# Kernel optimization log

Hardware: AMD Instinct MI355X
Metric: run time of the kernel (lower is better)

The kernel has to match this reference:

```python
import jax, jax.numpy as jnp
import numpy as np

B, IMG, P, D, E, K, H = 32, 224, 16, 512, 8, 2, 8
G = IMG // P
T = G * G          # 196 patches
PD = P * P         # 256 patch dim
FF = 4 * D         # expert hidden

def _posenc(t, d):
    pos = jnp.arange(t, dtype=jnp.float32)[:, None]
    i = jnp.arange(0, d, 2, dtype=jnp.float32)
    ang = pos / jnp.power(10000.0, i / d)
    pe = jnp.zeros((t, d), jnp.float32)
    pe = pe.at[:, 0::2].set(jnp.sin(ang))
    pe = pe.at[:, 1::2].set(jnp.cos(ang))
    return pe

def _attn(x, Wq, Wk, Wv, Wo, bo):
    bs, t, d = x.shape
    hs = d // H
    q = (x @ Wq).reshape(bs, t, H, hs).transpose(0, 2, 1, 3)
    k = (x @ Wk).reshape(bs, t, H, hs).transpose(0, 2, 1, 3)
    v = (x @ Wv).reshape(bs, t, H, hs).transpose(0, 2, 1, 3)
    wei = jnp.einsum('bhqd,bhkd->bhqk', q, k) * (hs ** -0.5)
    mask = jnp.tril(jnp.ones((t, t), dtype=bool))
    wei = jax.nn.softmax(jnp.where(mask, wei, -jnp.inf), axis=-1)
    o = jnp.einsum('bhqk,bhkd->bhqd', wei, v).transpose(0, 2, 1, 3).reshape(bs, t, d)
    return o @ Wo + bo

def _router(x, Wt, bt, Wn, bn, noise):
    # NoisyTopkRouter: noisy logits, top-k scatter to -inf background, softmax
    logits = x @ Wt + bt
    noisy = logits + noise * jax.nn.softplus(x @ Wn + bn)
    _, topi = jax.lax.top_k(noisy, K)
    sel = jax.nn.one_hot(topi, E, dtype=jnp.float32).sum(-2) > 0  # [B,T,E] bool
    return jax.nn.softmax(jnp.where(sel, noisy, -jnp.inf), axis=-1)

def _moe(x, gate, Wi, bi, Wo, bo):
    # gate is exactly zero off the top-k set, so dense all-expert compute
    # weighted by gate equals the original masked gather/scatter-add combine.
    h = jax.nn.relu(jnp.einsum('btd,edh->bteh', x, Wi) + bi)
    y = jnp.einsum('bteh,ehd->bted', h, Wo) + bo
    return jnp.einsum('bte,bted->btd', gate, y)

def _ln(x, g, b):
    mu = x.mean(-1, keepdims=True)
    var = ((x - mu) ** 2).mean(-1, keepdims=True)
    return (x - mu) / jnp.sqrt(var + 1e-5) * g + b

def _moe_layer(x, pW, pb, Wq, Wk, Wv, Wo, bo, rtW, rtb, rnW, rnb, eWi, ebi, eWo, ebo, lng, lnb, noise):
    x = x @ pW + pb                       # input_projection
    x = _attn(x, Wq, Wk, Wv, Wo, bo)      # multi-head causal self-attention
    gate = _router(x, rtW, rtb, rnW, rnb, noise)
    y = _moe(x, gate, eWi, ebi, eWo, ebo)
    return _ln(y, lng, lnb)               # dropout is identity in eval

def setup_inputs():
    key = jax.random.key(0)
    shapes = {"x": (B, 1, IMG, IMG), "pemb_W": (PD, D), "pemb_b": (D,), "vec_W": (D, D), "vec_b": (D,), "cls_W": (D, D), "cls_b": (D,)}
    for l in ("1", "2"):
        shapes.update({f"p{l}_W": (D, D), f"p{l}_b": (D,), f"Wq{l}": (D, D), f"Wk{l}": (D, D), f"Wv{l}": (D, D), f"Wo{l}": (D, D), f"bo{l}": (D,), f"rt{l}_W": (D, E), f"rt{l}_b": (E,), f"rn{l}_W": (D, E), f"rn{l}_b": (E,), f"eWi{l}": (E, D, FF), f"ebi{l}": (E, FF), f"eWo{l}": (E, FF, D), f"ebo{l}": (E, D), f"ln{l}_g": (D,), f"ln{l}_b": (D,), f"noise{l}": (B, T, E)})
    out = {}
    for i, (name, shp) in enumerate(shapes.items()):
        k = jax.random.fold_in(key, i)
        if name.startswith("ln") and name.endswith("_g"):
            out[name] = jnp.ones(shp, jnp.float32)
        else:
            scale = 1.0 if name == "x" or name.startswith("noise") else 0.02
            out[name] = jax.random.normal(k, shp, jnp.float32) * scale
    return out

def reference(x, pemb_W, pemb_b, vec_W, vec_b, cls_W, cls_b, p1_W, p1_b, Wq1, Wk1, Wv1, Wo1, bo1, rt1_W, rt1_b, rn1_W, rn1_b, eWi1, ebi1, eWo1, ebo1, ln1_g, ln1_b, noise1, p2_W, p2_b, Wq2, Wk2, Wv2, Wo2, bo2, rt2_W, rt2_b, rn2_W, rn2_b, eWi2, ebi2, eWo2, ebo2, ln2_g, ln2_b, noise2):
    bs = x.shape[0]
    # patchify (c==1): [B,1,IMG,IMG] -> [B,T,PD]
    patches = x[:, 0].reshape(bs, G, P, G, P).transpose(0, 1, 3, 2, 4).reshape(bs, T, PD)
    h = patches @ pemb_W + pemb_b + _posenc(T, D)[None]
    f1 = _moe_layer(h, p1_W, p1_b, Wq1, Wk1, Wv1, Wo1, bo1, rt1_W, rt1_b, rn1_W, rn1_b, eWi1, ebi1, eWo1, ebo1, ln1_g, ln1_b, noise1)
    first_vector = f1 @ vec_W + vec_b
    f2 = _moe_layer(first_vector, p2_W, p2_b, Wq2, Wk2, Wv2, Wo2, bo2, rt2_W, rt2_b, rn2_W, rn2_b, eWi2, ebi2, eWo2, ebo2, ln2_g, ln2_b, noise2)
    second_vector = f2 @ vec_W + vec_b
    # source bug: second_attn_weights is None; treated as uniform ones ->
    # mean over dim1 of ones is 1, so global = sum over patches.
    global_vector = second_vector.sum(axis=1)
    cls_vector = global_vector @ cls_W + cls_b
    return first_vector, second_vector, global_vector, cls_vector
```

## Files before the change

### kernel.cpp

```cpp
#include <hip/hip_runtime.h>

#define BT 6272
#define TT 196
#define DM 512
#define FFD 2048
#define NE 8
#define ABUF 3211264
#define SLOTS 12544

typedef float f32x4 __attribute__((ext_vector_type(4)));
typedef __bf16 bf16x8 __attribute__((ext_vector_type(8)));

__device__ __forceinline__ ushort f2bf(float f){
  union { float f; unsigned u; } v; v.f = f;
  unsigned u = v.u;
  u += 0x7fffu + ((u >> 16) & 1u);
  return (ushort)(u >> 16);
}
__device__ __forceinline__ float bf2f(ushort u){
  union { unsigned u; float f; } c; c.u = ((unsigned)u) << 16; return c.f;
}
__device__ __forceinline__ void splitbf(float v, ushort& hi, ushort& lo){
  union { float f; unsigned u; } c; c.f = v;
  hi = (ushort)(c.u >> 16);
  union { unsigned u; float f; } hf; hf.u = c.u & 0xffff0000u;
  lo = f2bf(v - hf.f);
}
__device__ __forceinline__ void glds16(const ushort* g, ushort* l){
  __builtin_amdgcn_global_load_lds(
      (const __attribute__((address_space(1))) unsigned int*)g,
      (__attribute__((address_space(3))) unsigned int*)l, 16, 0, 0);
}

__global__ void patchify_k(const float* __restrict__ x, ushort* __restrict__ oh, ushort* __restrict__ ol){
  int bt = blockIdx.x;
  int t = bt % TT, b = bt / TT;
  int pd = threadIdx.x;
  int g1 = t / 14, g2 = t % 14, p1 = pd >> 4, p2 = pd & 15;
  int src = (b*224 + g1*16 + p1)*224 + g2*16 + p2;
  float v = x[src];
  ushort hu, lu; splitbf(v, hu, lu);
  oh[(size_t)bt*256 + pd] = hu;
  ol[(size_t)bt*256 + pd] = lu;
}

__global__ void posenc_k(float* __restrict__ pe){
  int t = blockIdx.x, c = threadIdx.x;
  int m2 = c & ~1;
  double ang = (double)t * pow(10000.0, -(double)m2 / 512.0);
  double vv = (c & 1) ? cos(ang) : sin(ang);
  pe[t*DM + c] = (float)vv;
}

__global__ __launch_bounds__(256)
void wsplit_k(const float* __restrict__ src, ushort* __restrict__ dh, ushort* __restrict__ dl,
              int R, int C){
  __shared__ float t[32][33];
  int c0 = blockIdx.x << 5, r0 = blockIdx.y << 5;
  int tx = threadIdx.x & 31, ty = threadIdx.x >> 5;
  #pragma unroll
  for (int i = 0; i < 32; i += 8)
    t[ty+i][tx] = src[(size_t)(r0+ty+i)*C + c0 + tx];
  __syncthreads();
  #pragma unroll
  for (int i = 0; i < 32; i += 8){
    float v = t[tx][ty+i];
    ushort hu, lu; splitbf(v, hu, lu);
    dh[(size_t)(c0+ty+i)*R + r0 + tx] = hu;
    dl[(size_t)(c0+ty+i)*R + r0 + tx] = lu;
  }
}

__global__ __launch_bounds__(256)
void wsplit4_k(const float* __restrict__ s0, const float* __restrict__ s1,
               const float* __restrict__ s2, const float* __restrict__ s3,
               ushort* __restrict__ dQkvH, ushort* __restrict__ dQkvL,
               ushort* __restrict__ dWoH, ushort* __restrict__ dWoL)
{
  int z = blockIdx.z;
  const float* src = (z==0)? s0 : (z==1)? s1 : (z==2)? s2 : s3;
  ushort* dh; ushort* dl;
  if (z == 3){ dh = dWoH; dl = dWoL; }
  else { dh = dQkvH + (size_t)z*DM*DM; dl = dQkvL + (size_t)z*DM*DM; }
  __shared__ float t[32][33];
  int c0 = blockIdx.x << 5, r0 = blockIdx.y << 5;
  int tx = threadIdx.x & 31, ty = threadIdx.x >> 5;
  #pragma unroll
  for (int i = 0; i < 32; i += 8)
    t[ty+i][tx] = src[(size_t)(r0+ty+i)*DM + c0 + tx];
  __syncthreads();
  #pragma unroll
  for (int i = 0; i < 32; i += 8){
    float v = t[tx][ty+i];
    ushort hu, lu; splitbf(v, hu, lu);
    dh[(size_t)(c0+ty+i)*DM + r0 + tx] = hu;
    dl[(size_t)(c0+ty+i)*DM + r0 + tx] = lu;
  }
}

__global__ void esplit_k(const float* __restrict__ src, ushort* __restrict__ dh, ushort* __restrict__ dl){
  int i = blockIdx.x*256 + threadIdx.x;
  ushort hu, lu; splitbf(src[i], hu, lu);
  dh[i] = hu; dl[i] = lu;
}

__global__ __launch_bounds__(256)
void bfold_k(const float* __restrict__ pb, const float* __restrict__ Wq,
             const float* __restrict__ Wk, const float* __restrict__ Wv,
             float* __restrict__ bf){
  int tid = threadIdx.x;
  int w = tid >> 6, lane = tid & 63;
  int n = blockIdx.x*4 + w;
  const float* W = (n < 512) ? Wq : (n < 1024) ? Wk : Wv;
  int c = n & 511;
  float s = 0.f;
  #pragma unroll
  for (int u = 0; u < 8; ++u){
    int d = (u<<6) + lane;
    s += pb[d] * W[(size_t)d*DM + c];
  }
  #pragma unroll
  for (int off = 32; off; off >>= 1) s += __shfl_xor(s, off, 64);
  if (lane == 0) bf[n] = s;
}

__global__ __launch_bounds__(256)
void gemm_s(const ushort* __restrict__ Ah, const ushort* __restrict__ Al,
            const ushort* __restrict__ Bh, const ushort* __restrict__ Bl,
            const float* __restrict__ bias, const float* __restrict__ pe,
            float* __restrict__ Cf, ushort* __restrict__ Ch, ushort* __restrict__ Cl,
            int N, int kld)
{
  __shared__ ushort Ahs[2*128*32];
  __shared__ ushort Als[2*128*32];
  __shared__ ushort Bhs[2*128*32];
  __shared__ ushort Bls[2*128*32];
  int tid = threadIdx.x;
  int row0 = blockIdx.y << 7, col0 = blockIdx.x << 7;
  int lane = tid & 63, w = tid >> 6;
  int wr = w >> 1, wc = w & 1;
  int fr = lane & 15, fu = lane >> 4;
  int srow = 16*w + (lane >> 2);
  int cs = ((lane & 3) ^ ((srow >> 1) & 3)) << 3;
  const ushort* gAh0 = Ah + (size_t)(row0 + srow) * kld + cs;
  const ushort* gAh1 = Ah + (size_t)(row0 + 64 + srow) * kld + cs;
  const ushort* gAl0 = Al + (size_t)(row0 + srow) * kld + cs;
  const ushort* gAl1 = Al + (size_t)(row0 + 64 + srow) * kld + cs;
  const ushort* gBh0 = Bh + (size_t)(col0 + srow) * kld + cs;
  const ushort* gBh1 = Bh + (size_t)(col0 + 64 + srow) * kld + cs;
  const ushort* gBl0 = Bl + (size_t)(col0 + srow) * kld + cs;
  const ushort* gBl1 = Bl + (size_t)(col0 + 64 + srow) * kld + cs;
  int lo0 = (16*w)*32, lo1 = (64+16*w)*32;
  glds16(gAh0, &Ahs[lo0]); glds16(gAh1, &Ahs[lo1]);
  glds16(gAl0, &Als[lo0]); glds16(gAl1, &Als[lo1]);
  glds16(gBh0, &Bhs[lo0]); glds16(gBh1, &Bhs[lo1]);
  glds16(gBl0, &Bls[lo0]); glds16(gBl1, &Bls[lo1]);
  f32x4 acc[4][4] = {};
  int cur = 0;
  for (int k0 = 0; k0 < kld; k0 += 32){
    __syncthreads();
    if (k0 + 32 < kld){
      int nb = (cur ^ 1) * (128*32);
      glds16(gAh0 + k0+32, &Ahs[nb+lo0]); glds16(gAh1 + k0+32, &Ahs[nb+lo1]);
      glds16(gAl0 + k0+32, &Als[nb+lo0]); glds16(gAl1 + k0+32, &Als[nb+lo1]);
      glds16(gBh0 + k0+32, &Bhs[nb+lo0]); glds16(gBh1 + k0+32, &Bhs[nb+lo1]);
      glds16(gBl0 + k0+32, &Bls[nb+lo0]); glds16(gBl1 + k0+32, &Bls[nb+lo1]);
    }
    int cb = cur * (128*32);
    bf16x8 ah[4], al[4];
    #pragma unroll
    for (int i = 0; i < 4; ++i){
      int Ra = (wr<<6) + (i<<4) + fr;
      int oa = cb + Ra*32 + ((fu ^ ((Ra>>1)&3))<<3);
      ah[i] = *(const bf16x8*)&Ahs[oa];
      al[i] = *(const bf16x8*)&Als[oa];
    }
    #pragma unroll
    for (int j = 0; j < 4; ++j){
      int Rb = (wc<<6) + (j<<4) + fr;
      int ob = cb + Rb*32 + ((fu ^ ((Rb>>1)&3))<<3);
      bf16x8 bh = *(const bf16x8*)&Bhs[ob];
      bf16x8 bl = *(const bf16x8*)&Bls[ob];
      #pragma unroll
      for (int i = 0; i < 4; ++i){
        acc[i][j] = __builtin_amdgcn_mfma_f32_16x16x32_bf16(ah[i], bh, acc[i][j], 0, 0, 0);
        acc[i][j] = __builtin_amdgcn_mfma_f32_16x16x32_bf16(al[i], bh, acc[i][j], 0, 0, 0);
        acc[i][j] = __builtin_amdgcn_mfma_f32_16x16x32_bf16(ah[i], bl, acc[i][j], 0, 0, 0);
      }
    }
    cur ^= 1;
  }
  int fq = lane >> 4;
  #pragma unroll
  for (int j = 0; j < 4; ++j){
    int col = col0 + (wc<<6) + (j<<4) + fr;
    float bv = bias ? bias[col] : 0.f;
    #pragma unroll
    for (int i = 0; i < 4; ++i){
      #pragma unroll
      for (int q = 0; q < 4; ++q){
        int rr = row0 + (wr<<6) + (i<<4) + (fq<<2) + q;
        float v = acc[i][j][q] + bv;
        if (pe) v += pe[(size_t)(rr % TT)*DM + col];
        size_t off = (size_t)rr*N + col;
        if (Cf) Cf[off] = v;
        if (Ch){
          ushort hu, lu; splitbf(v, hu, lu);
          Ch[off] = hu; Cl[off] = lu;
        }
      }
    }
  }
}

__global__ __launch_bounds__(256)
void gemm_f32(const float* __restrict__ A, const float* __restrict__ Bw,
              float* __restrict__ C, const float* __restrict__ bias,
              float* __restrict__ obf, int M, int N, int K)
{
  __shared__ float As[16][68];
  __shared__ float Bs[16][68];
  int tid = threadIdx.x;
  int row0 = blockIdx.y << 6, col0 = blockIdx.x << 6;
  int ar = tid >> 2, ak = (tid & 3) << 2;
  int bk = tid >> 4, bn = (tid & 15) << 2;
  int n0 = (tid & 15) << 2, m0 = (tid >> 4) << 2;
  float acc[4][4] = {};
  bool arow_ok = (row0 + ar) < M;
  const float* Aldg = A + (size_t)(row0 + ar) * K + ak;
  const float* Bldg = Bw + (size_t)bk * N + col0 + bn;
  for (int k0 = 0; k0 < K; k0 += 16){
    float4 av = make_float4(0.f,0.f,0.f,0.f);
    if (arow_ok) av = *(const float4*)(Aldg + k0);
    float4 bv = *(const float4*)(Bldg + (size_t)k0 * N);
    __syncthreads();
    As[ak+0][ar]=av.x; As[ak+1][ar]=av.y; As[ak+2][ar]=av.z; As[ak+3][ar]=av.w;
    *(float4*)&Bs[bk][bn] = bv;
    __syncthreads();
    #pragma unroll
    for (int kk = 0; kk < 16; ++kk){
      float4 a = *(const float4*)&As[kk][m0];
      float4 b = *(const float4*)&Bs[kk][n0];
      float aa[4] = {a.x,a.y,a.z,a.w};
      float bb[4] = {b.x,b.y,b.z,b.w};
      #pragma unroll
      for (int i = 0; i < 4; ++i)
        #pragma unroll
        for (int j = 0; j < 4; ++j)
          acc[i][j] += aa[i]*bb[j];
    }
  }
  float4 badd = make_float4(0.f,0.f,0.f,0.f);
  if (bias) badd = *(const float4*)(bias + col0 + n0);
  #pragma unroll
  for (int i = 0; i < 4; ++i){
    int gr = row0 + m0 + i;
    if (gr < M){
      float4 r = make_float4(acc[i][0]+badd.x, acc[i][1]+badd.y, acc[i][2]+badd.z, acc[i][3]+badd.w);
      *(float4*)(C + (size_t)gr*N + col0 + n0) = r;
      if (obf) *(float4*)(obf + (size_t)gr*N + col0 + n0) = r;
    }
  }
}

__global__ __launch_bounds__(256)
void fattn_k(const ushort* __restrict__ Xh, const ushort* __restrict__ Xl,
             ushort* __restrict__ oh, ushort* __restrict__ ol)
{
  __shared__ ushort Kh[64][72], Kl[64][72];
  __shared__ ushort Vth[64][72], Vtl[64][72];
  __shared__ ushort Ph[64][72], Pl[64][72];
  int qt = blockIdx.x, bh = blockIdx.y;
  int b = bh >> 3, h = bh & 7;
  int tid = threadIdx.x;
  int w = tid >> 6, lane = tid & 63;
  int fr = lane & 15, fu = lane >> 4;
  int qrow_f = qt*64 + w*16 + fr;
  int qtok = b*TT + (qrow_f < TT ? qrow_f : TT-1);
  const ushort* qph = Xh + (size_t)qtok*1536 + h*64 + fu*8;
  const ushort* qpl = Xl + (size_t)qtok*1536 + h*64 + fu*8;
  bf16x8 qh0 = *(const bf16x8*)(qph);
  bf16x8 qh1 = *(const bf16x8*)(qph + 32);
  bf16x8 ql0 = *(const bf16x8*)(qpl);
  bf16x8 ql1 = *(const bf16x8*)(qpl + 32);
  f32x4 o_acc[4] = {};
  float m_i[4], l_i[4];
  #pragma unroll
  for (int q = 0; q < 4; ++q){ m_i[q] = -3e38f; l_i[q] = 0.f; }
  int sr = tid >> 2, sc = (tid & 3) << 4;
  int ktiles = qt + 1;
  for (int kt = 0; kt < ktiles; ++kt){
    __syncthreads();
    {
      int jrow = kt*64 + sr;
      int jtok = b*TT + (jrow < TT ? jrow : TT-1);
      const ushort* kph = Xh + (size_t)jtok*1536 + 512 + h*64 + sc;
      const ushort* kpl = Xl + (size_t)jtok*1536 + 512 + h*64 + sc;
      *(uint4*)&Kh[sr][sc]   = *(const uint4*)kph;
      *(uint4*)&Kh[sr][sc+8] = *(const uint4*)(kph + 8);
      *(uint4*)&Kl[sr][sc]   = *(const uint4*)kpl;
      *(uint4*)&Kl[sr][sc+8] = *(const uint4*)(kpl + 8);
      const ushort* vph = Xh + (size_t)jtok*1536 + 1024 + h*64 + sc;
      const ushort* vpl = Xl + (size_t)jtok*1536 + 1024 + h*64 + sc;
      ushort tv[16];
      *(uint4*)&tv[0] = *(const uint4*)vph;
      *(uint4*)&tv[8] = *(const uint4*)(vph + 8);
      #pragma unroll
      for (int t = 0; t < 16; ++t) Vth[sc + t][sr] = tv[t];
      *(uint4*)&tv[0] = *(const uint4*)vpl;
      *(uint4*)&tv[8] = *(const uint4*)(vpl + 8);
      #pragma unroll
      for (int t = 0; t < 16; ++t) Vtl[sc + t][sr] = tv[t];
    }
    __syncthreads();
    f32x4 sacc[4] = {};
    #pragma unroll
    for (int j = 0; j < 4; ++j){
      bf16x8 kh0 = *(const bf16x8*)&Kh[j*16 + fr][fu*8];
      bf16x8 kh1 = *(const bf16x8*)&Kh[j*16 + fr][32 + fu*8];
      bf16x8 kl0 = *(const bf16x8*)&Kl[j*16 + fr][fu*8];
      bf16x8 kl1 = *(const bf16x8*)&Kl[j*16 + fr][32 + fu*8];
      sacc[j] = __builtin_amdgcn_mfma_f32_16x16x32_bf16(qh0, kh0, sacc[j], 0, 0, 0);
      sacc[j] = __builtin_amdgcn_mfma_f32_16x16x32_bf16(ql0, kh0, sacc[j], 0, 0, 0);
      sacc[j] = __builtin_amdgcn_mfma_f32_16x16x32_bf16(qh0, kl0, sacc[j], 0, 0, 0);
      sacc[j] = __builtin_amdgcn_mfma_f32_16x16x32_bf16(qh1, kh1, sacc[j], 0, 0, 0);
      sacc[j] = __builtin_amdgcn_mfma_f32_16x16x32_bf16(ql1, kh1, sacc[j], 0, 0, 0);
      sacc[j] = __builtin_amdgcn_mfma_f32_16x16x32_bf16(qh1, kl1, sacc[j], 0, 0, 0);
    }
    int rbase = qt*64 + w*16 + (fu<<2);
    int cg = kt*64 + fr;
    float p[4][4];
    #pragma unroll
    for (int q = 0; q < 4; ++q){
      int rg = rbase + q;
      float sv[4];
      #pragma unroll
      for (int j = 0; j < 4; ++j){
        int cj = cg + j*16;
        sv[j] = (cj <= rg && cj < TT) ? sacc[j][q]*0.125f : -3e38f;
      }
      float mx = fmaxf(fmaxf(sv[0],sv[1]), fmaxf(sv[2],sv[3]));
      #pragma unroll
      for (int off = 1; off < 16; off <<= 1) mx = fmaxf(mx, __shfl_xor(mx, off, 64));
      float mnew = fmaxf(m_i[q], mx);
      float al = expf(m_i[q] - mnew);
      l_i[q] *= al;
      o_acc[0][q] *= al; o_acc[1][q] *= al; o_acc[2][q] *= al; o_acc[3][q] *= al;
      float ps = 0.f;
      #pragma unroll
      for (int j = 0; j < 4; ++j){ p[q][j] = expf(sv[j] - mnew); ps += p[q][j]; }
      #pragma unroll
      for (int off = 1; off < 16; off <<= 1) ps += __shfl_xor(ps, off, 64);
      l_i[q] += ps;
      m_i[q] = mnew;
    }
    #pragma unroll
    for (int q = 0; q < 4; ++q){
      int pr = w*16 + (fu<<2) + q;
      #pragma unroll
      for (int j = 0; j < 4; ++j){
        ushort hu, lu; splitbf(p[q][j], hu, lu);
        Ph[pr][j*16 + fr] = hu;
        Pl[pr][j*16 + fr] = lu;
      }
    }
    bf16x8 ph0 = *(const bf16x8*)&Ph[w*16 + fr][fu*8];
    bf16x8 ph1 = *(const bf16x8*)&Ph[w*16 + fr][32 + fu*8];
    bf16x8 pl0 = *(const bf16x8*)&Pl[w*16 + fr][fu*8];
    bf16x8 pl1 = *(const bf16x8*)&Pl[w*16 + fr][32 + fu*8];
    #pragma unroll
    for (int jd = 0; jd < 4; ++jd){
      bf16x8 vh0 = *(const bf16x8*)&Vth[jd*16 + fr][fu*8];
      bf16x8 vh1 = *(const bf16x8*)&Vth[jd*16 + fr][32 + fu*8];
      bf16x8 vl0 = *(const bf16x8*)&Vtl[jd*16 + fr][fu*8];
      bf16x8 vl1 = *(const bf16x8*)&Vtl[jd*16 + fr][32 + fu*8];
      o_acc[jd] = __builtin_amdgcn_mfma_f32_16x16x32_bf16(ph0, vh0, o_acc[jd], 0, 0, 0);
      o_acc[jd] = __builtin_amdgcn_mfma_f32_16x16x32_bf16(pl0, vh0, o_acc[jd], 0, 0, 0);
      o_acc[jd] = __builtin_amdgcn_mfma_f32_16x16x32_bf16(ph0, vl0, o_acc[jd], 0, 0, 0);
      o_acc[jd] = __builtin_amdgcn_mfma_f32_16x16x32_bf16(ph1, vh1, o_acc[jd], 0, 0, 0);
      o_acc[jd] = __builtin_amdgcn_mfma_f32_16x16x32_bf16(pl1, vh1, o_acc[jd], 0, 0, 0);
      o_acc[jd] = __builtin_amdgcn_mfma_f32_16x16x32_bf16(ph1, vl1, o_acc[jd], 0, 0, 0);
    }
  }
  #pragma unroll
  for (int q = 0; q < 4; ++q){
    int rg = qt*64 + w*16 + (fu<<2) + q;
    if (rg < TT){
      float inv = 1.f / l_i[q];
      size_t rowoff = (size_t)(b*TT + rg)*DM + h*64 + fr;
      #pragma unroll
      for (int jd = 0; jd < 4; ++jd){
        float v = o_acc[jd][q] * inv;
        ushort hu, lu; splitbf(v, hu, lu);
        oh[rowoff + jd*16] = hu;
        ol[rowoff + jd*16] = lu;
      }
    }
  }
}

__global__ __launch_bounds__(256)
void router2_k(const ushort* __restrict__ Xh, const ushort* __restrict__ Xl,
               const float* __restrict__ rtW, const float* __restrict__ rtb,
               const float* __restrict__ rnW, const float* __restrict__ rnb, const float* __restrict__ nz,
               int* __restrict__ tok_e, float* __restrict__ tok_g)
{
  __shared__ float Wt[8*513];
  __shared__ float Wn[8*513];
  int tid = threadIdx.x;
  for (int i = tid*4; i < DM*8; i += 1024){
    float4 t = *(const float4*)(rtW + i);
    float4 n = *(const float4*)(rnW + i);
    int d = i >> 3, e = i & 7;
    Wt[(e+0)*513 + d] = t.x; Wt[(e+1)*513 + d] = t.y; Wt[(e+2)*513 + d] = t.z; Wt[(e+3)*513 + d] = t.w;
    Wn[(e+0)*513 + d] = n.x; Wn[(e+1)*513 + d] = n.y; Wn[(e+2)*513 + d] = n.z; Wn[(e+3)*513 + d] = n.w;
  }
  __syncthreads();
  int w = tid >> 6, lane = tid & 63;
  int t = (blockIdx.x << 2) + w;
  const ushort* xh = Xh + (size_t)t * DM;
  const ushort* xl = Xl + (size_t)t * DM;
  float at[8] = {}, an[8] = {};
  #pragma unroll
  for (int u = 0; u < 8; ++u){
    int d = (u<<6) + lane;
    float xv = bf2f(xh[d]) + bf2f(xl[d]);
    #pragma unroll
    for (int e = 0; e < 8; ++e){
      at[e] += xv * Wt[e*513 + d];
      an[e] += xv * Wn[e*513 + d];
    }
  }
  #pragma unroll
  for (int off = 32; off; off >>= 1){
    #pragma unroll
    for (int e = 0; e < 8; ++e){
      at[e] += __shfl_xor(at[e], off, 64);
      an[e] += __shfl_xor(an[e], off, 64);
    }
  }
  if (lane == 0){
    float ns[8];
    #pragma unroll
    for (int e = 0; e < 8; ++e){
      float lt = at[e] + rtb[e];
      float ln_ = an[e] + rnb[e];
      float sp = (ln_ > 0.f) ? (ln_ + log1pf(expf(-ln_))) : log1pf(expf(ln_));
      ns[e] = lt + nz[(size_t)t*8 + e] * sp;
    }
    int i1 = 0; float n1 = ns[0];
    #pragma unroll
    for (int e = 1; e < 8; ++e) if (ns[e] > n1){ n1 = ns[e]; i1 = e; }
    int i2 = -1; float n2 = -3e38f;
    #pragma unroll
    for (int e = 0; e < 8; ++e) if (e != i1 && ns[e] > n2){ n2 = ns[e]; i2 = e; }
    float ex = expf(n2 - n1);
    float inv = 1.f / (1.f + ex);
    tok_e[t*2]   = i1; tok_g[t*2]   = inv;
    tok_e[t*2+1] = i2; tok_g[t*2+1] = ex * inv;
  }
}

__global__ __launch_bounds__(1024)
void route_assign_k(const int* __restrict__ tok_e, int* __restrict__ offs_g,
                    int* __restrict__ idx_c, int* __restrict__ tok_slot)
{
  __shared__ int hist[NE];
  __shared__ int cur[NE];
  int tid = threadIdx.x;
  if (tid < NE) hist[tid] = 0;
  __syncthreads();
  for (int i = tid; i < BT*2; i += 1024) atomicAdd(&hist[tok_e[i]], 1);
  __syncthreads();
  if (tid == 0){
    int s = 0;
    for (int e = 0; e < NE; ++e){ offs_g[e] = s; cur[e] = s; s += hist[e]; }
    offs_g[NE] = s;
  }
  __syncthreads();
  for (int i = tid; i < BT*2; i += 1024){
    int e = tok_e[i];
    int p = atomicAdd(&cur[e], 1);
    idx_c[p] = i >> 1;
    tok_slot[i] = p;
  }
}

__global__ __launch_bounds__(256)
void transconv_k(const float* __restrict__ src, ushort* __restrict__ dst, int R, int C){
  __shared__ float t[32][33];
  int e = blockIdx.z;
  src += (size_t)e * R * C;
  dst += (size_t)e * R * C;
  int c0 = blockIdx.x << 5, r0 = blockIdx.y << 5;
  int tx = threadIdx.x & 31, ty = threadIdx.x >> 5;
  #pragma unroll
  for (int i = 0; i < 32; i += 8)
    t[ty+i][tx] = src[(size_t)(r0+ty+i)*C + c0 + tx];
  __syncthreads();
  #pragma unroll
  for (int i = 0; i < 32; i += 8)
    dst[(size_t)(c0+ty+i)*R + r0 + tx] = f2bf(t[tx][ty+i]);
}

__global__ void gatherconv_k(const ushort* __restrict__ Xh, const int* __restrict__ idx,
                             ushort* __restrict__ Xg){
  int s = blockIdx.x;
  const ushort* xp = Xh + (size_t)idx[s] * DM;
  ushort* op = Xg + (size_t)s * DM;
  int i = threadIdx.x * 2;
  *(ushort2*)(op + i) = *(const ushort2*)(xp + i);
}

template<int MODE>
__global__ __launch_bounds__(256)
void moe_mfma(const ushort* __restrict__ A, const ushort* __restrict__ Bt,
              const float* __restrict__ bias, const int* __restrict__ offs,
              void* __restrict__ Out, int kld, int ldb, int out_ld, int accum)
{
  int e = blockIdx.z;
  int base = offs[e], cnt = offs[e+1] - base;
  int row0 = blockIdx.y << 7;
  if (row0 >= cnt) return;
  int col0 = blockIdx.x << 7;
  __shared__ ushort As[2*128*32];
  __shared__ ushort Bs[2*128*32];
  int tid = threadIdx.x, lane = tid & 63, w = tid >> 6;
  int wr = w >> 1, wc = w & 1;
  int fr = lane & 15, fu = lane >> 4;
  int srow = 16*w + (lane >> 2);
  int cs = ((lane & 3) ^ ((srow >> 1) & 3)) << 3;
  int ar0 = base + row0 + srow;      if (ar0 > SLOTS-1) ar0 = SLOTS-1;
  int ar1 = base + row0 + 64 + srow; if (ar1 > SLOTS-1) ar1 = SLOTS-1;
  const ushort* gA0 = A + (size_t)ar0 * kld + cs;
  const ushort* gA1 = A + (size_t)ar1 * kld + cs;
  const ushort* Bb = Bt + (size_t)e * ((size_t)FFD*DM);
  const ushort* gB0 = Bb + (size_t)(col0 + srow) * ldb + cs;
  const ushort* gB1 = Bb + (size_t)(col0 + 64 + srow) * ldb + cs;
  int lo0 = (16*w)*32, lo1 = (64+16*w)*32;
  glds16(gA0, &As[lo0]); glds16(gA1, &As[lo1]);
  glds16(gB0, &Bs[lo0]); glds16(gB1, &Bs[lo1]);
  f32x4 acc[4][4] = {};
  int cur = 0;
  for (int k0 = 0; k0 < kld; k0 += 32){
    __syncthreads();
    if (k0 + 32 < kld){
      int nb = (cur ^ 1) * (128*32);
      glds16(gA0 + k0+32, &As[nb+lo0]); glds16(gA1 + k0+32, &As[nb+lo1]);
      glds16(gB0 + k0+32, &Bs[nb+lo0]); glds16(gB1 + k0+32, &Bs[nb+lo1]);
    }
    int cb = cur * (128*32);
    bf16x8 af[4], bf[4];
    #pragma unroll
    for (int i = 0; i < 4; ++i){
      int Ra = (wr<<6) + (i<<4) + fr;
      af[i] = *(const bf16x8*)&As[cb + Ra*32 + ((fu ^ ((Ra>>1)&3))<<3)];
      int Rb = (wc<<6) + (i<<4) + fr;
      bf[i] = *(const bf16x8*)&Bs[cb + Rb*32 + ((fu ^ ((Rb>>1)&3))<<3)];
    }
    #pragma unroll
    for (int i = 0; i < 4; ++i)
      #pragma unroll
      for (int j = 0; j < 4; ++j)
        acc[i][j] = __builtin_amdgcn_mfma_f32_16x16x32_bf16(af[i], bf[j], acc[i][j], 0, 0, 0);
    cur ^= 1;
  }
  int fq = lane >> 4;
  #pragma unroll
  for (int j = 0; j < 4; ++j){
    int col = col0 + (wc<<6) + (j<<4) + fr;
    float bv = bias[(size_t)e * ((MODE==0)?FFD:DM) + col];
    #pragma unroll
    for (int i = 0; i < 4; ++i){
      #pragma unroll
      for (int q = 0; q < 4; ++q){
        int rr = row0 + (wr<<6) + (i<<4) + (fq<<2) + q;
        if (rr < cnt){
          if (MODE == 0){
            float vv = acc[i][j][q] + bv;
            ((ushort*)Out)[(size_t)(base+rr)*out_ld + col] = f2bf(fmaxf(vv, 0.f));
          } else {
            float* yp = (float*)Out + (size_t)(base+rr)*out_ld + col;
            *yp = acc[i][j][q] + (accum ? *yp : bv);
          }
        }
      }
    }
  }
}

__global__ __launch_bounds__(256)
void combine_ln_k(const float* __restrict__ Ye, const int* __restrict__ tok_slot,
                  const float* __restrict__ tok_g, const float* __restrict__ g,
                  const float* __restrict__ bb, ushort* __restrict__ oh, ushort* __restrict__ ol)
{
  int t = blockIdx.x, tid = threadIdx.x;
  int s1 = tok_slot[t*2], s2 = tok_slot[t*2+1];
  float g1 = tok_g[t*2], g2 = tok_g[t*2+1];
  const float* y1 = Ye + (size_t)s1*DM;
  const float* y2 = Ye + (size_t)s2*DM;
  float v0 = g1*y1[tid]     + g2*y2[tid];
  float v1 = g1*y1[tid+256] + g2*y2[tid+256];
  __shared__ float red[8];
  int w = tid >> 6, lane = tid & 63;
  float s = v0 + v1;
  #pragma unroll
  for (int off = 32; off; off >>= 1) s += __shfl_xor(s, off, 64);
  if (lane == 0) red[w] = s;
  __syncthreads();
  float mu = (red[0]+red[1]+red[2]+red[3]) * (1.f/512.f);
  float d0 = v0 - mu, d1 = v1 - mu;
  float q2 = d0*d0 + d1*d1;
  #pragma unroll
  for (int off = 32; off; off >>= 1) q2 += __shfl_xor(q2, off, 64);
  if (lane == 0) red[4+w] = q2;
  __syncthreads();
  float var = (red[4]+red[5]+red[6]+red[7]) * (1.f/512.f);
  float r = 1.f / sqrtf(var + 1e-5f);
  float r0v = d0*r*g[tid]     + bb[tid];
  float r1v = d1*r*g[tid+256] + bb[tid+256];
  ushort hu, lu;
  splitbf(r0v, hu, lu);
  oh[(size_t)t*DM + tid] = hu; ol[(size_t)t*DM + tid] = lu;
  splitbf(r1v, hu, lu);
  oh[(size_t)t*DM + tid + 256] = hu; ol[(size_t)t*DM + tid + 256] = lu;
}

__global__ void gsum_k(const float* __restrict__ sv, float* __restrict__ gb, float* __restrict__ gout){
  int i = blockIdx.x*256 + threadIdx.x;
  int b = i >> 9, d = i & 511;
  const float* p = sv + (size_t)b*TT*DM + d;
  float s = 0.f;
  for (int t = 0; t < TT; ++t) s += p[(size_t)t*DM];
  gb[i] = s; gout[i] = s;
}

extern "C" void kernel_launch(void* const* d_in, const int* in_sizes, int n_in,
                              void* d_out, int out_size, void* d_ws, size_t ws_size,
                              hipStream_t stream)
{
  (void)in_sizes; (void)n_in; (void)out_size;
  const float* xin   = (const float*)d_in[0];
  const float* pembW = (const float*)d_in[1];
  const float* pembB = (const float*)d_in[2];
  const float* vecW  = (const float*)d_in[3];
  const float* vecB  = (const float*)d_in[4];
  const float* clsW  = (const float*)d_in[5];
  const float* clsB  = (const float*)d_in[6];
  float* out = (float*)d_out;

  const size_t QKV_SH  = (size_t)2*BT*1536;
  const size_t RMIN_SH = QKV_SH + (size_t)2*1536*DM + (size_t)2*DM*DM;
  const size_t FIXF =
      (size_t)SLOTS*DM
    + (size_t)2*ABUF
    + (size_t)SLOTS*DM/2
    + (size_t)NE*FFD*DM
    + (size_t)256*DM
    + (size_t)DM*DM
    + (size_t)3*DM*DM
    + (size_t)DM*DM
    + (size_t)TT*DM + 2048
    + 16384*2 + SLOTS + SLOTS*3 + 64;
  int fcw = 256;
  for (int cand = 2048; cand >= 256; cand >>= 1){
    size_t reg_sh = (size_t)SLOTS*cand > RMIN_SH ? (size_t)SLOTS*cand : RMIN_SH;
    size_t need = (FIXF + reg_sh/2) * sizeof(float);
    if (need <= ws_size){ fcw = cand; break; }
  }
  size_t region_sh = (size_t)SLOTS*fcw > RMIN_SH ? (size_t)SLOTS*fcw : RMIN_SH;

  float* ws = (float*)d_ws;
  float* Yexp = ws;
  ushort* S0h = (ushort*)(Yexp + (size_t)SLOTS*DM);
  ushort* S0l = S0h + ABUF;
  ushort* S1h = S0l + ABUF;
  ushort* S1l = S1h + ABUF;
  ushort* region = S1l + ABUF;
  ushort* Xg   = region + region_sh;
  ushort* WiT  = Xg + (size_t)SLOTS*DM;
  ushort* WoT  = WiT + (size_t)NE*FFD*DM;
  ushort* PembH = WoT + (size_t)NE*FFD*DM;
  ushort* PembL = PembH + 256*DM;
  ushort* VecH = PembL + 256*DM;
  ushort* VecL = VecH + DM*DM;
  ushort* QkvWH = VecL + DM*DM;
  ushort* QkvWL = QkvWH + 3*DM*DM;
  ushort* WoSH = QkvWL + 3*DM*DM;
  ushort* WoSL = WoSH + DM*DM;
  float* pe    = (float*)(WoSL + DM*DM);
  float* bfold = pe + TT*DM;
  float* gbv   = bfold + 2048;
  float* clsbuf= gbv + 16384;
  float* tok_g = clsbuf + 16384;
  int* tok_e   = (int*)(tok_g + SLOTS);
  int* tok_slot= tok_e + SLOTS;
  int* idx_c   = tok_slot + SLOTS;
  int* offs    = idx_c + SLOTS;
  ushort* QKVh = region;
  ushort* QKVl = region + (size_t)BT*1536;
  ushort* FoldWH = region + QKV_SH;
  ushort* FoldWL = FoldWH + (size_t)1536*DM;
  ushort* PWh  = FoldWL + (size_t)1536*DM;
  ushort* PWl  = PWh + (size_t)DM*DM;
  ushort* H1b  = region;
  ushort* PATh = region;
  ushort* PATl = region + (size_t)BT*256;

  patchify_k<<<dim3(BT), dim3(256), 0, stream>>>(xin, PATh, PATl);
  posenc_k<<<dim3(TT), dim3(512), 0, stream>>>(pe);
  wsplit_k<<<dim3(16, 8), dim3(256), 0, stream>>>(pembW, PembH, PembL, 256, DM);
  wsplit_k<<<dim3(16, 16), dim3(256), 0, stream>>>(vecW, VecH, VecL, DM, DM);
  gemm_s<<<dim3(4,49), dim3(256), 0, stream>>>(PATh, PATl, PembH, PembL, pembB, pe,
                                               nullptr, S0h, S0l, DM, 256);

  ushort *INh = S0h, *INl = S0l, *TPh = S1h, *TPl = S1l;
  for (int l = 0; l < 2; ++l){
    int base = 7 + 18*l;
    const float* pW  = (const float*)d_in[base+0];
    const float* pb  = (const float*)d_in[base+1];
    const float* Wq  = (const float*)d_in[base+2];
    const float* Wk  = (const float*)d_in[base+3];
    const float* Wv  = (const float*)d_in[base+4];
    const float* Wo  = (const float*)d_in[base+5];
    const float* bo  = (const float*)d_in[base+6];
    const float* rtW = (const float*)d_in[base+7];
    const float* rtb = (const float*)d_in[base+8];
    const float* rnW = (const float*)d_in[base+9];
    const float* rnb = (const float*)d_in[base+10];
    const float* eWi = (const float*)d_in[base+11];
    const float* ebi = (const float*)d_in[base+12];
    const float* eWo = (const float*)d_in[base+13];
    const float* ebo = (const float*)d_in[base+14];
    const float* lng = (const float*)d_in[base+15];
    const float* lnb = (const float*)d_in[base+16];
    const float* nz  = (const float*)d_in[base+17];

    wsplit4_k<<<dim3(16,16,4), dim3(256), 0, stream>>>(Wq, Wk, Wv, Wo,
                                                       QkvWH, QkvWL, WoSH, WoSL);
    esplit_k<<<dim3(1024), dim3(256), 0, stream>>>(pW, PWh, PWl);
    gemm_s<<<dim3(4,12), dim3(256), 0, stream>>>(QkvWH, QkvWL, PWh, PWl, nullptr, nullptr,
                                                 nullptr, FoldWH, FoldWL, DM, DM);
    bfold_k<<<dim3(384), dim3(256), 0, stream>>>(pb, Wq, Wk, Wv, bfold);
    gemm_s<<<dim3(12,49), dim3(256), 0, stream>>>(INh, INl, FoldWH, FoldWL, bfold, nullptr,
                                                 nullptr, QKVh, QKVl, 1536, DM);
    fattn_k<<<dim3(4,256), dim3(256), 0, stream>>>(QKVh, QKVl, INh, INl);
    gemm_s<<<dim3(4,49), dim3(256), 0, stream>>>(INh, INl, WoSH, WoSL, bo, nullptr,
                                                 nullptr, TPh, TPl, DM, DM);
    transconv_k<<<dim3(FFD/32, DM/32, NE), dim3(256), 0, stream>>>(eWi, WiT, DM, FFD);
    transconv_k<<<dim3(DM/32, FFD/32, NE), dim3(256), 0, stream>>>(eWo, WoT, FFD, DM);
    router2_k<<<dim3(BT/4), dim3(256), 0, stream>>>(TPh, TPl, rtW, rtb, rnW, rnb, nz, tok_e, tok_g);
    route_assign_k<<<dim3(1), dim3(1024), 0, stream>>>(tok_e, offs, idx_c, tok_slot);
    gatherconv_k<<<dim3(SLOTS), dim3(256), 0, stream>>>(TPh, idx_c, Xg);
    for (int c0 = 0; c0 < FFD; c0 += fcw){
      moe_mfma<0><<<dim3(fcw/128, 49, NE), dim3(256), 0, stream>>>(
          Xg, WiT + (size_t)c0*DM, ebi + c0, offs, (void*)H1b, DM, DM, fcw, 0);
      moe_mfma<1><<<dim3(DM/128, 49, NE), dim3(256), 0, stream>>>(
          H1b, WoT + c0, ebo, offs, (void*)Yexp, fcw, FFD, DM, c0);
    }
    combine_ln_k<<<dim3(BT), dim3(256), 0, stream>>>(Yexp, tok_slot, tok_g, lng, lnb, INh, INl);
    gemm_s<<<dim3(4,49), dim3(256), 0, stream>>>(INh, INl, VecH, VecL, vecB, nullptr,
                                                 out + (size_t)l*ABUF, TPh, TPl, DM, DM);
    ushort* th = INh; INh = TPh; TPh = th;
    ushort* tl = INl; INl = TPl; TPl = tl;
  }

  gsum_k<<<dim3(64), dim3(256), 0, stream>>>(out + ABUF, gbv, out + 2*ABUF);
  gemm_f32<<<dim3(8,1), dim3(256), 0, stream>>>(gbv, clsW, clsbuf, clsB, out + 2*ABUF + 16384, 32, DM, DM);
}
```

Measured before the change: 1.091 ms.

## Pipeline GEMM loads, swizzle workgroups across XCDs, fuse gather and transposes

Several unrelated changes land together. The gemm_s and moe_mfma loops prefetch two stages ahead and use explicit vmcnt waits with raw barriers instead of one __syncthreads per k step. Workgroup IDs are remapped so neighbouring tiles land on the same XCD for L2 reuse. The separate gather kernel is removed: the first MoE GEMM reads token rows directly through the index array. The two expert-weight transpose launches become one, and route assignment uses wave-aggregated ballot atomics. The hand-written vmcnt counts must match the number of outstanding loads per stage, and the gathered global loads may coalesce less well.

```diff
diff --git a/kernel.cpp b/kernel.cpp
--- a/kernel.cpp
+++ b/kernel.cpp
@@ -30,6 +30,11 @@
   __builtin_amdgcn_global_load_lds(
       (const __attribute__((address_space(1))) unsigned int*)g,
       (__attribute__((address_space(3))) unsigned int*)l, 16, 0, 0);
+}
+__device__ __forceinline__ int xcd_swz(int f, int nwg){
+  int q = nwg >> 3, r = nwg & 7;
+  int xcd = f & 7, i = f >> 3;
+  return (xcd < r ? xcd*(q+1) : r*(q+1) + (xcd-r)*q) + i;
 }
 
 __global__ void patchify_k(const float* __restrict__ x, ushort* __restrict__ oh, ushort* __restrict__ ol){
@@ -135,8 +140,12 @@
   __shared__ ushort Als[2*128*32];
   __shared__ ushort Bhs[2*128*32];
   __shared__ ushort Bls[2*128*32];
+  int gx = gridDim.x, gy = gridDim.y;
+  int fblk = blockIdx.x + gx*blockIdx.y;
+  int wgt = xcd_swz(fblk, gx*gy);
+  int bx = wgt % gx, by = wgt / gx;
+  int row0 = by << 7, col0 = bx << 7;
   int tid = threadIdx.x;
-  int row0 = blockIdx.y << 7, col0 = blockIdx.x << 7;
   int lane = tid & 63, w = tid >> 6;
   int wr = w >> 1, wc = w & 1;
   int fr = lane & 15, fu = lane >> 4;
@@ -151,22 +160,21 @@
   const ushort* gBl0 = Bl + (size_t)(col0 + srow) * kld + cs;
   const ushort* gBl1 = Bl + (size_t)(col0 + 64 + srow) * kld + cs;
   int lo0 = (16*w)*32, lo1 = (64+16*w)*32;
-  glds16(gAh0, &Ahs[lo0]); glds16(gAh1, &Ahs[lo1]);
-  glds16(gAl0, &Als[lo0]); glds16(gAl1, &Als[lo1]);
-  glds16(gBh0, &Bhs[lo0]); glds16(gBh1, &Bhs[lo1]);
-  glds16(gBl0, &Bls[lo0]); glds16(gBl1, &Bls[lo1]);
+  #define GSTAGE(koff, nb) { \
+    glds16(gAh0 + (koff), &Ahs[(nb)+lo0]); glds16(gAh1 + (koff), &Ahs[(nb)+lo1]); \
+    glds16(gAl0 + (koff), &Als[(nb)+lo0]); glds16(gAl1 + (koff), &Als[(nb)+lo1]); \
+    glds16(gBh0 + (koff), &Bhs[(nb)+lo0]); glds16(gBh1 + (koff), &Bhs[(nb)+lo1]); \
+    glds16(gBl0 + (koff), &Bls[(nb)+lo0]); glds16(gBl1 + (koff), &Bls[(nb)+lo1]); }
   f32x4 acc[4][4] = {};
-  int cur = 0;
-  for (int k0 = 0; k0 < kld; k0 += 32){
-    __syncthreads();
-    if (k0 + 32 < kld){
-      int nb = (cur ^ 1) * (128*32);
-      glds16(gAh0 + k0+32, &Ahs[nb+lo0]); glds16(gAh1 + k0+32, &Ahs[nb+lo1]);
-      glds16(gAl0 + k0+32, &Als[nb+lo0]); glds16(gAl1 + k0+32, &Als[nb+lo1]);
-      glds16(gBh0 + k0+32, &Bhs[nb+lo0]); glds16(gBh1 + k0+32, &Bhs[nb+lo1]);
-      glds16(gBl0 + k0+32, &Bls[nb+lo0]); glds16(gBl1 + k0+32, &Bls[nb+lo1]);
-    }
-    int cb = cur * (128*32);
+  int nt = kld >> 5;
+  GSTAGE(0, 0)
+  GSTAGE(32, 128*32)
+  for (int t = 0; t < nt; ++t){
+    if (t + 1 < nt) asm volatile("s_waitcnt vmcnt(8)" ::: "memory");
+    else            asm volatile("s_waitcnt vmcnt(0)" ::: "memory");
+    __builtin_amdgcn_s_barrier();
+    __builtin_amdgcn_sched_barrier(0);
+    int cb = (t & 1) * (128*32);
     bf16x8 ah[4], al[4];
     #pragma unroll
     for (int i = 0; i < 4; ++i){
@@ -188,8 +196,12 @@
         acc[i][j] = __builtin_amdgcn_mfma_f32_16x16x32_bf16(ah[i], bl, acc[i][j], 0, 0, 0);
       }
     }
-    cur ^= 1;
-  }
+    __builtin_amdgcn_sched_barrier(0);
+    __builtin_amdgcn_s_barrier();
+    __builtin_amdgcn_sched_barrier(0);
+    if (t + 2 < nt) GSTAGE((t+2) << 5, (t & 1) * (128*32))
+  }
+  #undef GSTAGE
   int fq = lane >> 4;
   #pragma unroll
   for (int j = 0; j < 4; ++j){
@@ -468,9 +480,17 @@
   __shared__ int hist[NE];
   __shared__ int cur[NE];
   int tid = threadIdx.x;
+  int lane = tid & 63;
   if (tid < NE) hist[tid] = 0;
   __syncthreads();
-  for (int i = tid; i < BT*2; i += 1024) atomicAdd(&hist[tok_e[i]], 1);
+  for (int i = tid; i < BT*2; i += 1024){
+    int e = tok_e[i];
+    #pragma unroll
+    for (int x = 0; x < NE; ++x){
+      unsigned long long m = __ballot(e == x);
+      if (m && lane == (int)__builtin_ctzll(m)) atomicAdd(&hist[x], __popcll(m));
+    }
+  }
   __syncthreads();
   if (tid == 0){
     int s = 0;
@@ -480,19 +500,37 @@
   __syncthreads();
   for (int i = tid; i < BT*2; i += 1024){
     int e = tok_e[i];
-    int p = atomicAdd(&cur[e], 1);
+    int p = 0;
+    #pragma unroll
+    for (int x = 0; x < NE; ++x){
+      unsigned long long m = __ballot(e == x);
+      if (m){
+        int leader = (int)__builtin_ctzll(m);
+        int bw = 0;
+        if (lane == leader) bw = atomicAdd(&cur[x], __popcll(m));
+        bw = __shfl(bw, leader, 64);
+        if (e == x) p = bw + __popcll(m & ((lane == 63) ? 0x7fffffffffffffffull : ((1ull << lane) - 1ull)));
+      }
+    }
     idx_c[p] = i >> 1;
     tok_slot[i] = p;
   }
 }
 
 __global__ __launch_bounds__(256)
-void transconv_k(const float* __restrict__ src, ushort* __restrict__ dst, int R, int C){
+void transconv2_k(const float* __restrict__ eWi, const float* __restrict__ eWo,
+                  ushort* __restrict__ WiT, ushort* __restrict__ WoT){
   __shared__ float t[32][33];
-  int e = blockIdx.z;
-  src += (size_t)e * R * C;
-  dst += (size_t)e * R * C;
-  int c0 = blockIdx.x << 5, r0 = blockIdx.y << 5;
+  int z = blockIdx.z;
+  const float* src; ushort* dst; int R, C, c0, r0;
+  if (z < NE){
+    src = eWi + (size_t)z*DM*FFD; dst = WiT + (size_t)z*DM*FFD;
+    R = DM; C = FFD; c0 = blockIdx.x << 5; r0 = blockIdx.y << 5;
+  } else {
+    int e = z - NE;
+    src = eWo + (size_t)e*FFD*DM; dst = WoT + (size_t)e*FFD*DM;
+    R = FFD; C = DM; c0 = blockIdx.y << 5; r0 = blockIdx.x << 5;
+  }
   int tx = threadIdx.x & 31, ty = threadIdx.x >> 5;
   #pragma unroll
   for (int i = 0; i < 32; i += 8)
@@ -503,26 +541,24 @@
     dst[(size_t)(c0+ty+i)*R + r0 + tx] = f2bf(t[tx][ty+i]);
 }
 
-__global__ void gatherconv_k(const ushort* __restrict__ Xh, const int* __restrict__ idx,
-                             ushort* __restrict__ Xg){
-  int s = blockIdx.x;
-  const ushort* xp = Xh + (size_t)idx[s] * DM;
-  ushort* op = Xg + (size_t)s * DM;
-  int i = threadIdx.x * 2;
-  *(ushort2*)(op + i) = *(const ushort2*)(xp + i);
-}
-
 template<int MODE>
 __global__ __launch_bounds__(256)
-void moe_mfma(const ushort* __restrict__ A, const ushort* __restrict__ Bt,
+void moe_mfma(const ushort* __restrict__ A, const int* __restrict__ aidx,
+              const ushort* __restrict__ Bt,
               const float* __restrict__ bias, const int* __restrict__ offs,
               void* __restrict__ Out, int kld, int ldb, int out_ld, int accum)
 {
-  int e = blockIdx.z;
+  int gx = gridDim.x, gy = gridDim.y;
+  int nwg = gx * gy * (int)gridDim.z;
+  int fblk = blockIdx.x + gx*(blockIdx.y + gy*blockIdx.z);
+  int wgt = xcd_swz(fblk, nwg);
+  int bx = wgt % gx; wgt /= gx;
+  int by = wgt % gy; int bz = wgt / gy;
+  int e = bz;
   int base = offs[e], cnt = offs[e+1] - base;
-  int row0 = blockIdx.y << 7;
+  int row0 = by << 7;
   if (row0 >= cnt) return;
-  int col0 = blockIdx.x << 7;
+  int col0 = bx << 7;
   __shared__ ushort As[2*128*32];
   __shared__ ushort Bs[2*128*32];
   int tid = threadIdx.x, lane = tid & 63, w = tid >> 6;
@@ -530,26 +566,29 @@
   int fr = lane & 15, fu = lane >> 4;
   int srow = 16*w + (lane >> 2);
   int cs = ((lane & 3) ^ ((srow >> 1) & 3)) << 3;
-  int ar0 = base + row0 + srow;      if (ar0 > SLOTS-1) ar0 = SLOTS-1;
-  int ar1 = base + row0 + 64 + srow; if (ar1 > SLOTS-1) ar1 = SLOTS-1;
-  const ushort* gA0 = A + (size_t)ar0 * kld + cs;
-  const ushort* gA1 = A + (size_t)ar1 * kld + cs;
+  int s0 = base + row0 + srow;      if (s0 > SLOTS-1) s0 = SLOTS-1;
+  int s1 = base + row0 + 64 + srow; if (s1 > SLOTS-1) s1 = SLOTS-1;
+  int r0i = (MODE == 0) ? aidx[s0] : s0;
+  int r1i = (MODE == 0) ? aidx[s1] : s1;
+  const ushort* gA0 = A + (size_t)r0i * kld + cs;
+  const ushort* gA1 = A + (size_t)r1i * kld + cs;
   const ushort* Bb = Bt + (size_t)e * ((size_t)FFD*DM);
   const ushort* gB0 = Bb + (size_t)(col0 + srow) * ldb + cs;
   const ushort* gB1 = Bb + (size_t)(col0 + 64 + srow) * ldb + cs;
   int lo0 = (16*w)*32, lo1 = (64+16*w)*32;
-  glds16(gA0, &As[lo0]); glds16(gA1, &As[lo1]);
-  glds16(gB0, &Bs[lo0]); glds16(gB1, &Bs[lo1]);
+  #define MSTAGE(koff, nb) { \
+    glds16(gA0 + (koff), &As[(nb)+lo0]); glds16(gA1 + (koff), &As[(nb)+lo1]); \
+    glds16(gB0 + (koff), &Bs[(nb)+lo0]); glds16(gB1 + (koff), &Bs[(nb)+lo1]); }
   f32x4 acc[4][4] = {};
-  int cur = 0;
-  for (int k0 = 0; k0 < kld; k0 += 32){
-    __syncthreads();
-    if (k0 + 32 < kld){
-      int nb = (cur ^ 1) * (128*32);
-      glds16(gA0 + k0+32, &As[nb+lo0]); glds16(gA1 + k0+32, &As[nb+lo1]);
-      glds16(gB0 + k0+32, &Bs[nb+lo0]); glds16(gB1 + k0+32, &Bs[nb+lo1]);
-    }
-    int cb = cur * (128*32);
+  int nt = kld >> 5;
+  MSTAGE(0, 0)
+  MSTAGE(32, 128*32)
+  for (int t = 0; t < nt; ++t){
+    if (t + 1 < nt) asm volatile("s_waitcnt vmcnt(4)" ::: "memory");
+    else            asm volatile("s_waitcnt vmcnt(0)" ::: "memory");
+    __builtin_amdgcn_s_barrier();
+    __builtin_amdgcn_sched_barrier(0);
+    int cb = (t & 1) * (128*32);
     bf16x8 af[4], bf[4];
     #pragma unroll
     for (int i = 0; i < 4; ++i){
@@ -563,8 +602,12 @@
       #pragma unroll
       for (int j = 0; j < 4; ++j)
         acc[i][j] = __builtin_amdgcn_mfma_f32_16x16x32_bf16(af[i], bf[j], acc[i][j], 0, 0, 0);
-    cur ^= 1;
-  }
+    __builtin_amdgcn_sched_barrier(0);
+    __builtin_amdgcn_s_barrier();
+    __builtin_amdgcn_sched_barrier(0);
+    if (t + 2 < nt) MSTAGE((t+2) << 5, (t & 1) * (128*32))
+  }
+  #undef MSTAGE
   int fq = lane >> 4;
   #pragma unroll
   for (int j = 0; j < 4; ++j){
@@ -654,7 +697,6 @@
   const size_t FIXF =
       (size_t)SLOTS*DM
     + (size_t)2*ABUF
-    + (size_t)SLOTS*DM/2
     + (size_t)NE*FFD*DM
     + (size_t)256*DM
     + (size_t)DM*DM
@@ -677,8 +719,7 @@
   ushort* S1h = S0l + ABUF;
   ushort* S1l = S1h + ABUF;
   ushort* region = S1l + ABUF;
-  ushort* Xg   = region + region_sh;
-  ushort* WiT  = Xg + (size_t)SLOTS*DM;
+  ushort* WiT  = region + region_sh;
   ushort* WoT  = WiT + (size_t)NE*FFD*DM;
   ushort* PembH = WoT + (size_t)NE*FFD*DM;
   ushort* PembL = PembH + 256*DM;
@@ -747,16 +788,14 @@
     fattn_k<<<dim3(4,256), dim3(256), 0, stream>>>(QKVh, QKVl, INh, INl);
     gemm_s<<<dim3(4,49), dim3(256), 0, stream>>>(INh, INl, WoSH, WoSL, bo, nullptr,
                                                  nullptr, TPh, TPl, DM, DM);
-    transconv_k<<<dim3(FFD/32, DM/32, NE), dim3(256), 0, stream>>>(eWi, WiT, DM, FFD);
-    transconv_k<<<dim3(DM/32, FFD/32, NE), dim3(256), 0, stream>>>(eWo, WoT, FFD, DM);
+    transconv2_k<<<dim3(64, 16, 2*NE), dim3(256), 0, stream>>>(eWi, eWo, WiT, WoT);
     router2_k<<<dim3(BT/4), dim3(256), 0, stream>>>(TPh, TPl, rtW, rtb, rnW, rnb, nz, tok_e, tok_g);
     route_assign_k<<<dim3(1), dim3(1024), 0, stream>>>(tok_e, offs, idx_c, tok_slot);
-    gatherconv_k<<<dim3(SLOTS), dim3(256), 0, stream>>>(TPh, idx_c, Xg);
     for (int c0 = 0; c0 < FFD; c0 += fcw){
       moe_mfma<0><<<dim3(fcw/128, 49, NE), dim3(256), 0, stream>>>(
-          Xg, WiT + (size_t)c0*DM, ebi + c0, offs, (void*)H1b, DM, DM, fcw, 0);
+          TPh, idx_c, WiT + (size_t)c0*DM, ebi + c0, offs, (void*)H1b, DM, DM, fcw, 0);
       moe_mfma<1><<<dim3(DM/128, 49, NE), dim3(256), 0, stream>>>(
-          H1b, WoT + c0, ebo, offs, (void*)Yexp, fcw, FFD, DM, c0);
+          H1b, nullptr, WoT + c0, ebo, offs, (void*)Yexp, fcw, FFD, DM, c0);
     }
     combine_ln_k<<<dim3(BT), dim3(256), 0, stream>>>(Yexp, tok_slot, tok_g, lng, lnb, INh, INl);
     gemm_s<<<dim3(4,49), dim3(256), 0, stream>>>(INh, INl, VecH, VecL, vecB, nullptr,
```

Result: no change. 1.071 ms (-1.9%).
